# Optimization experiments

Measured on AMD Instinct MI355X. Metric: run time of the kernel, lower is better.

## Reference

```python
import jax, jax.numpy as jnp
import numpy as np

N, E, D, H = 50000, 800000, 128, 8
DH = D // H  # 16
EPS_LN = 1e-5


def layer_norm(x, gamma, beta):
    mu = jnp.mean(x, axis=-1, keepdims=True)
    var = jnp.var(x, axis=-1, keepdims=True)
    return (x - mu) * jax.lax.rsqrt(var + EPS_LN) * gamma + beta


def setup_inputs() -> dict:
    key = jax.random.key(0)
    ks = jax.random.split(key, 12)
    s = 1.0 / np.sqrt(D)
    x = jax.random.normal(ks[0], (N, D), dtype=jnp.float32)
    src = jax.random.randint(ks[1], (E,), 0, N, dtype=jnp.int32)
    dst = jax.random.randint(ks[2], (E,), 0, N, dtype=jnp.int32)
    Wq = jax.random.normal(ks[3], (D, D), dtype=jnp.float32) * s
    Wk = jax.random.normal(ks[4], (D, D), dtype=jnp.float32) * s
    Wv = jax.random.normal(ks[5], (D, D), dtype=jnp.float32) * s
    Wo = jax.random.normal(ks[6], (D, D), dtype=jnp.float32) * s
    bq = jnp.zeros((D,), jnp.float32)
    bk = jnp.zeros((D,), jnp.float32)
    bv = jnp.zeros((D,), jnp.float32)
    bo = jnp.zeros((D,), jnp.float32)
    gamma1 = jnp.ones((D,), jnp.float32)
    beta1 = jnp.zeros((D,), jnp.float32)
    gamma2 = jnp.ones((D,), jnp.float32)
    beta2 = jnp.zeros((D,), jnp.float32)
    return dict(x=x, src=src, dst=dst, Wq=Wq, bq=bq, Wk=Wk, bk=bk, Wv=Wv, bv=bv,
                Wo=Wo, bo=bo, gamma1=gamma1, beta1=beta1, gamma2=gamma2, beta2=beta2)


def reference(x, src, dst, Wq, bq, Wk, bk, Wv, bv, Wo, bo, gamma1, beta1, gamma2, beta2):
    n = x.shape[0]
    Q = (x @ Wq + bq).reshape(n, H, DH)   # [N,H,Dh]
    K = (x @ Wk + bk).reshape(n, H, DH)
    V = (x @ Wv + bv).reshape(n, H, DH)
    # edge-wise QK dot: score[e,h] = sum_d K[src[e],h,d] * Q[dst[e],h,d]
    score = jnp.sum(K[src] * Q[dst], axis=-1) / np.sqrt(DH)  # [E,H]
    score = jnp.exp(jnp.clip(score, -5.0, 5.0))
    # scatter-sum weighted values and normalizer over destination nodes
    wV = jax.ops.segment_sum(V[src] * score[..., None], dst, num_segments=n)  # [N,H,Dh]
    z = jax.ops.segment_sum(score, dst, num_segments=n)                        # [N,H]
    attn = (wV / (z[..., None] + 1e-3)).reshape(n, D)
    h = layer_norm(x + attn, gamma1, beta1)
    # sublayer: h + relu(O(LN(h)))  (dropout = 0)
    h = h + jax.nn.relu(layer_norm(h, gamma2, beta2) @ Wo + bo)
    return h
```

## Files before the change

### kernel.cpp

```cpp
#include <hip/hip_runtime.h>
#include <hip/hip_bf16.h>

typedef unsigned short ushort_t;
typedef __attribute__((ext_vector_type(8))) short short8;
typedef __attribute__((ext_vector_type(4))) float floatx4;

__device__ __forceinline__ unsigned short f2bf(float f) {
    union { float f; unsigned u; } x; x.f = f;
    unsigned r = x.u + 0x7fffu + ((x.u >> 16) & 1u);
    return (unsigned short)(r >> 16);
}
__device__ __forceinline__ float bf2f(unsigned short u) {
    union { unsigned u; float f; } x; x.u = ((unsigned)u) << 16; return x.f;
}
__device__ __forceinline__ float u2f(unsigned u) {
    union { unsigned u; float f; } x; x.u = u; return x.f;
}

__global__ __launch_bounds__(256) void transpose128(
    const float* __restrict__ Wq, const float* __restrict__ Wk,
    const float* __restrict__ Wv, const float* __restrict__ Wo,
    ushort_t* __restrict__ out)
{
    const float* W = (blockIdx.y == 0) ? Wq : (blockIdx.y == 1) ? Wk :
                     (blockIdx.y == 2) ? Wv : Wo;
    ushort_t* T = out + (size_t)blockIdx.y * 128 * 128;
    int tr = blockIdx.x >> 2, tc = blockIdx.x & 3;
    __shared__ float s[32][33];
    int tx = threadIdx.x & 31, ty = threadIdx.x >> 5;
    for (int j = 0; j < 32; j += 8)
        s[ty + j][tx] = W[(tr * 32 + ty + j) * 128 + tc * 32 + tx];
    __syncthreads();
    for (int j = 0; j < 32; j += 8)
        T[(tc * 32 + ty + j) * 128 + tr * 32 + tx] = f2bf(s[tx][ty + j]);
}

__global__ __launch_bounds__(256) void gemm_qkv(
    const float* __restrict__ X, const ushort_t* __restrict__ Wt,
    const float* __restrict__ bq, const float* __restrict__ bk, const float* __restrict__ bv,
    ushort_t* __restrict__ Q, ushort_t* __restrict__ KV, int M,
    const int* __restrict__ dst, int* __restrict__ deg, int E)
{
    __shared__ ushort_t Xs[64 * 136];
    __shared__ ushort_t Ws[128 * 136];
    int tid = threadIdx.x;
    int rowBase = blockIdx.x * 64;
    int wsel = blockIdx.y;
    const ushort_t* Wmat = Wt + (size_t)wsel * 128 * 128;
    const float* bias = (wsel == 0) ? bq : (wsel == 1) ? bk : bv;

    {
        int nblk = gridDim.x * gridDim.y;
        int fb = blockIdx.y * gridDim.x + blockIdx.x;
        int per = (E + nblk - 1) / nblk;
        int end = min(per * (fb + 1), E);
        for (int i = per * fb + tid; i < end; i += 256)
            atomicAdd(&deg[dst[i]], 1);
    }

    int r = tid >> 4;
    int c = (tid & 15) * 8;
    for (int rr = 0; rr < 64; rr += 16) {
        int row = rowBase + rr + r;
        int rc = (row < M) ? row : (M - 1);
        const float* p = X + (size_t)rc * 128 + c;
        float4 f0 = *(const float4*)p;
        float4 f1 = *(const float4*)(p + 4);
        short8 v;
        v[0] = (short)f2bf(f0.x); v[1] = (short)f2bf(f0.y);
        v[2] = (short)f2bf(f0.z); v[3] = (short)f2bf(f0.w);
        v[4] = (short)f2bf(f1.x); v[5] = (short)f2bf(f1.y);
        v[6] = (short)f2bf(f1.z); v[7] = (short)f2bf(f1.w);
        *(short8*)&Xs[(rr + r) * 136 + c] = v;
    }
    for (int rr = 0; rr < 128; rr += 16) {
        short8 v = *(const short8*)(Wmat + (size_t)(rr + r) * 128 + c);
        *(short8*)&Ws[(rr + r) * 136 + c] = v;
    }
    __syncthreads();

    int lane = tid & 63, wave = tid >> 6;
    int wm = wave * 16;
    int l15 = lane & 15, quad = lane >> 4;
    floatx4 acc[8] = {};
    for (int k0 = 0; k0 < 128; k0 += 32) {
        short8 a = *(const short8*)&Xs[(wm + l15) * 136 + k0 + quad * 8];
        for (int sn = 0; sn < 8; sn++) {
            short8 b = *(const short8*)&Ws[(sn * 16 + l15) * 136 + k0 + quad * 8];
            acc[sn] = __builtin_amdgcn_mfma_f32_16x16x32_bf16(a, b, acc[sn], 0, 0, 0);
        }
    }
    for (int sn = 0; sn < 8; sn++) {
        int col = sn * 16 + l15;
        float bia = bias[col];
        for (int rr2 = 0; rr2 < 4; rr2++) {
            int row = rowBase + wm + quad * 4 + rr2;
            if (row < M) {
                ushort_t val = f2bf(acc[sn][rr2] + bia);
                if (wsel == 0) {
                    Q[(size_t)row * 128 + col] = val;
                } else {
                    size_t idx = (size_t)row * 256 + ((col >> 3) << 4) + (col & 7) + ((wsel == 2) ? 8 : 0);
                    KV[idx] = val;
                }
            }
        }
    }
}

__global__ __launch_bounds__(256) void k_scan_blocks(const int* __restrict__ deg, int* __restrict__ offs,
                                                     int* __restrict__ bsums, int n) {
    __shared__ int s[256];
    int i = blockIdx.x * 256 + threadIdx.x;
    int v = (i < n) ? deg[i] : 0;
    s[threadIdx.x] = v;
    __syncthreads();
    for (int d = 1; d < 256; d <<= 1) {
        int t = (threadIdx.x >= d) ? s[threadIdx.x - d] : 0;
        __syncthreads();
        s[threadIdx.x] += t;
        __syncthreads();
    }
    int incl = s[threadIdx.x];
    if (i < n) offs[i] = incl - v;
    if (threadIdx.x == 255) bsums[blockIdx.x] = incl;
}

__global__ __launch_bounds__(256) void k_add_base(int* __restrict__ offs, int* __restrict__ cursor,
                                                  const int* __restrict__ bs, int nb, int n, int E) {
    int tid = threadIdx.x;
    int acc = 0;
    for (int t = tid; t < nb; t += 256)
        if (t < (int)blockIdx.x) acc += bs[t];
    for (int m = 1; m < 64; m <<= 1) acc += __shfl_xor(acc, m, 64);
    __shared__ int sw[4];
    if ((tid & 63) == 0) sw[tid >> 6] = acc;
    __syncthreads();
    int base = sw[0] + sw[1] + sw[2] + sw[3];
    int i = blockIdx.x * 256 + tid;
    if (i < n) {
        int o = offs[i] + base;
        offs[i] = o;
        cursor[i] = o;
    }
    if (blockIdx.x == 0 && tid == 0) offs[n] = E;
}

__global__ __launch_bounds__(256) void k_scatter(const int* __restrict__ src, const int* __restrict__ dst,
                                                 int* __restrict__ cursor, int* __restrict__ eadj, int E) {
    int i = blockIdx.x * 256 + threadIdx.x;
    if (i < E) {
        int p = atomicAdd(&cursor[dst[i]], 1);
        eadj[p] = src[i];
    }
}

__global__ __launch_bounds__(256) void edge_attn(
    const ushort_t* __restrict__ Qb, const ushort_t* __restrict__ KV,
    const float* __restrict__ xin,
    const int* __restrict__ offs, const int* __restrict__ eadj,
    const float* __restrict__ g1, const float* __restrict__ be1,
    const float* __restrict__ g2, const float* __restrict__ be2,
    ushort_t* __restrict__ h1out, ushort_t* __restrict__ ln2out, int N)
{
    int wave = threadIdx.x >> 6, lane = threadIdx.x & 63;
    int n = blockIdx.x * 4 + wave;
    if (n >= N) return;
    int l15 = lane & 15, grp = lane >> 4;

    uint4 qp = *(const uint4*)(Qb + (size_t)n * 128 + l15 * 8);
    float q0 = u2f(qp.x << 16), q1 = u2f(qp.x & 0xffff0000u);
    float q2 = u2f(qp.y << 16), q3 = u2f(qp.y & 0xffff0000u);
    float q4 = u2f(qp.z << 16), q5 = u2f(qp.z & 0xffff0000u);
    float q6 = u2f(qp.w << 16), q7 = u2f(qp.w & 0xffff0000u);

    int s0 = offs[n], s1 = offs[n + 1];
    float a0=0.f,a1=0.f,a2=0.f,a3=0.f,a4=0.f,a5=0.f,a6=0.f,a7=0.f,z=0.f;
    for (int base = s0; base < s1; base += 64) {
        int cnt = min(s1 - base, 64);
        int ee = (base + lane < s1) ? eadj[base + lane] : 0;
        #pragma unroll 2
        for (int j = 0; j < cnt; j += 4) {
            int jj = j + grp;
            int sn = __shfl(ee, jj, 64);
            const ushort_t* kvp = KV + (size_t)sn * 256 + l15 * 16;
            uint4 kk = *(const uint4*)kvp;
            uint4 vv = *(const uint4*)(kvp + 8);
            float d = q0 * u2f(kk.x << 16) + q1 * u2f(kk.x & 0xffff0000u)
                    + q2 * u2f(kk.y << 16) + q3 * u2f(kk.y & 0xffff0000u)
                    + q4 * u2f(kk.z << 16) + q5 * u2f(kk.z & 0xffff0000u)
                    + q6 * u2f(kk.w << 16) + q7 * u2f(kk.w & 0xffff0000u);
            d += __shfl_xor(d, 1, 64);
            float sc = fminf(5.f, fmaxf(-5.f, d * 0.25f));
            float e = (jj < cnt) ? __expf(sc) : 0.f;
            a0 = fmaf(e, u2f(vv.x << 16), a0); a1 = fmaf(e, u2f(vv.x & 0xffff0000u), a1);
            a2 = fmaf(e, u2f(vv.y << 16), a2); a3 = fmaf(e, u2f(vv.y & 0xffff0000u), a3);
            a4 = fmaf(e, u2f(vv.z << 16), a4); a5 = fmaf(e, u2f(vv.z & 0xffff0000u), a5);
            a6 = fmaf(e, u2f(vv.w << 16), a6); a7 = fmaf(e, u2f(vv.w & 0xffff0000u), a7);
            z += e;
        }
    }
    a0 += __shfl_xor(a0, 16, 64); a0 += __shfl_xor(a0, 32, 64);
    a1 += __shfl_xor(a1, 16, 64); a1 += __shfl_xor(a1, 32, 64);
    a2 += __shfl_xor(a2, 16, 64); a2 += __shfl_xor(a2, 32, 64);
    a3 += __shfl_xor(a3, 16, 64); a3 += __shfl_xor(a3, 32, 64);
    a4 += __shfl_xor(a4, 16, 64); a4 += __shfl_xor(a4, 32, 64);
    a5 += __shfl_xor(a5, 16, 64); a5 += __shfl_xor(a5, 32, 64);
    a6 += __shfl_xor(a6, 16, 64); a6 += __shfl_xor(a6, 32, 64);
    a7 += __shfl_xor(a7, 16, 64); a7 += __shfl_xor(a7, 32, 64);
    z  += __shfl_xor(z, 16, 64);  z  += __shfl_xor(z, 32, 64);
    float inv = 1.f / (z + 1e-3f);

    const float* xr = xin + (size_t)n * 128 + l15 * 8;
    float4 xa = *(const float4*)xr;
    float4 xb = *(const float4*)(xr + 4);
    float t0 = xa.x + a0 * inv, t1 = xa.y + a1 * inv;
    float t2 = xa.z + a2 * inv, t3 = xa.w + a3 * inv;
    float t4 = xb.x + a4 * inv, t5 = xb.y + a5 * inv;
    float t6 = xb.z + a6 * inv, t7 = xb.w + a7 * inv;

    float s  = t0 + t1 + t2 + t3 + t4 + t5 + t6 + t7;
    float s2 = t0*t0 + t1*t1 + t2*t2 + t3*t3 + t4*t4 + t5*t5 + t6*t6 + t7*t7;
    for (int m = 1; m < 16; m <<= 1) { s += __shfl_xor(s, m, 64); s2 += __shfl_xor(s2, m, 64); }
    float mu = s * (1.f / 128.f);
    float var = s2 * (1.f / 128.f) - mu * mu;
    float rstd = rsqrtf(var + 1e-5f);

    const float* g1r = g1 + l15 * 8;
    const float* b1r = be1 + l15 * 8;
    float4 ga = *(const float4*)g1r, gb = *(const float4*)(g1r + 4);
    float4 ba = *(const float4*)b1r, bb = *(const float4*)(b1r + 4);
    float h0 = (t0 - mu) * rstd * ga.x + ba.x;
    float h1 = (t1 - mu) * rstd * ga.y + ba.y;
    float h2 = (t2 - mu) * rstd * ga.z + ba.z;
    float h3 = (t3 - mu) * rstd * ga.w + ba.w;
    float h4 = (t4 - mu) * rstd * gb.x + bb.x;
    float h5 = (t5 - mu) * rstd * gb.y + bb.y;
    float h6 = (t6 - mu) * rstd * gb.z + bb.z;
    float h7 = (t7 - mu) * rstd * gb.w + bb.w;
    if (grp == 0) {
        uint4 pk;
        pk.x = (unsigned)f2bf(h0) | ((unsigned)f2bf(h1) << 16);
        pk.y = (unsigned)f2bf(h2) | ((unsigned)f2bf(h3) << 16);
        pk.z = (unsigned)f2bf(h4) | ((unsigned)f2bf(h5) << 16);
        pk.w = (unsigned)f2bf(h6) | ((unsigned)f2bf(h7) << 16);
        *(uint4*)(h1out + (size_t)n * 128 + l15 * 8) = pk;
    }

    s  = h0 + h1 + h2 + h3 + h4 + h5 + h6 + h7;
    s2 = h0*h0 + h1*h1 + h2*h2 + h3*h3 + h4*h4 + h5*h5 + h6*h6 + h7*h7;
    for (int m = 1; m < 16; m <<= 1) { s += __shfl_xor(s, m, 64); s2 += __shfl_xor(s2, m, 64); }
    float mu2 = s * (1.f / 128.f);
    float var2 = s2 * (1.f / 128.f) - mu2 * mu2;
    float rstd2 = rsqrtf(var2 + 1e-5f);

    const float* g2r = g2 + l15 * 8;
    const float* b2r = be2 + l15 * 8;
    float4 gc = *(const float4*)g2r, gd = *(const float4*)(g2r + 4);
    float4 bc = *(const float4*)b2r, bd = *(const float4*)(b2r + 4);
    float l0 = (h0 - mu2) * rstd2 * gc.x + bc.x;
    float l1 = (h1 - mu2) * rstd2 * gc.y + bc.y;
    float l2 = (h2 - mu2) * rstd2 * gc.z + bc.z;
    float l3 = (h3 - mu2) * rstd2 * gc.w + bc.w;
    float l4 = (h4 - mu2) * rstd2 * gd.x + bd.x;
    float l5 = (h5 - mu2) * rstd2 * gd.y + bd.y;
    float l6 = (h6 - mu2) * rstd2 * gd.z + bd.z;
    float l7 = (h7 - mu2) * rstd2 * gd.w + bd.w;
    if (grp == 1) {
        uint4 pk;
        pk.x = (unsigned)f2bf(l0) | ((unsigned)f2bf(l1) << 16);
        pk.y = (unsigned)f2bf(l2) | ((unsigned)f2bf(l3) << 16);
        pk.z = (unsigned)f2bf(l4) | ((unsigned)f2bf(l5) << 16);
        pk.w = (unsigned)f2bf(l6) | ((unsigned)f2bf(l7) << 16);
        *(uint4*)(ln2out + (size_t)n * 128 + l15 * 8) = pk;
    }
}

__global__ __launch_bounds__(256) void gemm_o(
    const ushort_t* __restrict__ X, const ushort_t* __restrict__ Wt,
    const float* __restrict__ bo, const ushort_t* __restrict__ h1in,
    float* __restrict__ Out, int M)
{
    __shared__ ushort_t As[64 * 136];
    __shared__ ushort_t Bs[64 * 136];
    int tid = threadIdx.x;
    int rowBase = blockIdx.x * 64;
    int colBase = blockIdx.y * 64;

    int r = tid >> 4;
    int c = (tid & 15) * 8;
    for (int rr = 0; rr < 64; rr += 16) {
        int row = rowBase + rr + r;
        int rc = (row < M) ? row : (M - 1);
        short8 v = *(const short8*)(X + (size_t)rc * 128 + c);
        *(short8*)&As[(rr + r) * 136 + c] = v;
    }
    for (int rr = 0; rr < 64; rr += 16) {
        short8 v = *(const short8*)(Wt + (size_t)(colBase + rr + r) * 128 + c);
        *(short8*)&Bs[(rr + r) * 136 + c] = v;
    }
    __syncthreads();

    int lane = tid & 63, wave = tid >> 6;
    int wm = (wave >> 1) * 32, wn = (wave & 1) * 32;
    int l15 = lane & 15, quad = lane >> 4;
    floatx4 acc[2][2] = {};
    for (int k0 = 0; k0 < 128; k0 += 32) {
        short8 a[2], b[2];
        for (int sm = 0; sm < 2; sm++)
            a[sm] = *(const short8*)&As[(wm + sm * 16 + l15) * 136 + k0 + quad * 8];
        for (int sn = 0; sn < 2; sn++)
            b[sn] = *(const short8*)&Bs[(wn + sn * 16 + l15) * 136 + k0 + quad * 8];
        for (int sm = 0; sm < 2; sm++)
            for (int sn = 0; sn < 2; sn++)
                acc[sm][sn] = __builtin_amdgcn_mfma_f32_16x16x32_bf16(a[sm], b[sn], acc[sm][sn], 0, 0, 0);
    }
    for (int sm = 0; sm < 2; sm++)
        for (int sn = 0; sn < 2; sn++) {
            int col = colBase + wn + sn * 16 + l15;
            float bia = bo[col];
            for (int rr2 = 0; rr2 < 4; rr2++) {
                int row = rowBase + wm + sm * 16 + quad * 4 + rr2;
                if (row < M) {
                    float v = fmaxf(acc[sm][sn][rr2] + bia, 0.f);
                    float hv = bf2f(h1in[(size_t)row * 128 + col]);
                    Out[(size_t)row * 128 + col] = hv + v;
                }
            }
        }
}

extern "C" void kernel_launch(void* const* d_in, const int* in_sizes, int n_in,
                              void* d_out, int out_size, void* d_ws, size_t ws_size,
                              hipStream_t stream) {
    const int D = 128;
    const int N = in_sizes[0] / D;
    const int E = in_sizes[1];

    const float* x   = (const float*)d_in[0];
    const int*   src = (const int*)d_in[1];
    const int*   dst = (const int*)d_in[2];
    const float* Wq  = (const float*)d_in[3];
    const float* bq  = (const float*)d_in[4];
    const float* Wk  = (const float*)d_in[5];
    const float* bk  = (const float*)d_in[6];
    const float* Wv  = (const float*)d_in[7];
    const float* bv  = (const float*)d_in[8];
    const float* Wo  = (const float*)d_in[9];
    const float* bo  = (const float*)d_in[10];
    const float* g1  = (const float*)d_in[11];
    const float* be1 = (const float*)d_in[12];
    const float* g2  = (const float*)d_in[13];
    const float* be2 = (const float*)d_in[14];

    char* ws = (char*)d_ws;
    size_t o = 0;
    auto alloc = [&](size_t b) { o = (o + 255) & ~(size_t)255; size_t r = o; o += b; return r; };
    ushort_t* Qb   = (ushort_t*)(ws + alloc((size_t)N * D * 2));
    ushort_t* KVb  = (ushort_t*)(ws + alloc((size_t)N * D * 4));
    ushort_t* ln2  = (ushort_t*)(ws + alloc((size_t)N * D * 2));
    ushort_t* h1   = (ushort_t*)(ws + alloc((size_t)N * D * 2));
    ushort_t* Wt   = (ushort_t*)(ws + alloc((size_t)4 * 128 * 128 * 2));
    int*      deg  = (int*)(ws + alloc((size_t)N * 4));
    int*      offs = (int*)(ws + alloc((size_t)(N + 1) * 4));
    int*      cur  = (int*)(ws + alloc((size_t)N * 4));
    int*      bsum = (int*)(ws + alloc((size_t)256 * 4));
    int*      eadj = (int*)(ws + alloc((size_t)E * 4));

    int nScanBlocks = (N + 255) / 256;
    int nEdgeBlocks = (E + 255) / 256;
    int nRowTiles = (N + 63) / 64;

    hipMemsetAsync(deg, 0, (size_t)N * 4, stream);
    transpose128<<<dim3(16, 4), 256, 0, stream>>>(Wq, Wk, Wv, Wo, Wt);
    gemm_qkv<<<dim3(nRowTiles, 3), 256, 0, stream>>>(x, Wt, bq, bk, bv, Qb, KVb, N, dst, deg, E);
    k_scan_blocks<<<nScanBlocks, 256, 0, stream>>>(deg, offs, bsum, N);
    k_add_base<<<nScanBlocks, 256, 0, stream>>>(offs, cur, bsum, nScanBlocks, N, E);
    k_scatter<<<nEdgeBlocks, 256, 0, stream>>>(src, dst, cur, eadj, E);
    edge_attn<<<(N + 3) / 4, 256, 0, stream>>>(Qb, KVb, x, offs, eadj, g1, be1, g2, be2, h1, ln2, N);
    gemm_o<<<dim3(nRowTiles, 2), 256, 0, stream>>>(ln2, Wt + 3 * 128 * 128, bo, h1, (float*)d_out, N);
}
```

Measured before the change: 280.6 us.

## Fuse edge attention, layer norms and output projection into one kernel

The edge attention kernel now processes 16 nodes per block (4 per wave), keeps h1 and LN2 rows in shared memory, and runs the Wo projection with MFMA directly from that tile before writing the final output. This drops the gemm_o launch and the global round trip of the bf16 h1 and ln2 buffers. Wo is read from global memory per block rather than staged, and the per-wave sequential node loop plus the block barrier may reduce latency hiding for the irregular gather. The QK dot product is also split into partial sums to shorten the dependency chain.

```diff
diff --git a/kernel.cpp b/kernel.cpp
--- a/kernel.cpp
+++ b/kernel.cpp
@@ -155,179 +155,159 @@
     }
 }
 
-__global__ __launch_bounds__(256) void edge_attn(
+__global__ __launch_bounds__(256) void attn_fused(
     const ushort_t* __restrict__ Qb, const ushort_t* __restrict__ KV,
     const float* __restrict__ xin,
     const int* __restrict__ offs, const int* __restrict__ eadj,
     const float* __restrict__ g1, const float* __restrict__ be1,
     const float* __restrict__ g2, const float* __restrict__ be2,
-    ushort_t* __restrict__ h1out, ushort_t* __restrict__ ln2out, int N)
+    const ushort_t* __restrict__ Wo_t, const float* __restrict__ bo,
+    float* __restrict__ Out, int N)
 {
+    __shared__ ushort_t ln2s[16 * 136];
+    __shared__ ushort_t h1s[16 * 136];
     int wave = threadIdx.x >> 6, lane = threadIdx.x & 63;
-    int n = blockIdx.x * 4 + wave;
-    if (n >= N) return;
     int l15 = lane & 15, grp = lane >> 4;
-
-    uint4 qp = *(const uint4*)(Qb + (size_t)n * 128 + l15 * 8);
-    float q0 = u2f(qp.x << 16), q1 = u2f(qp.x & 0xffff0000u);
-    float q2 = u2f(qp.y << 16), q3 = u2f(qp.y & 0xffff0000u);
-    float q4 = u2f(qp.z << 16), q5 = u2f(qp.z & 0xffff0000u);
-    float q6 = u2f(qp.w << 16), q7 = u2f(qp.w & 0xffff0000u);
-
-    int s0 = offs[n], s1 = offs[n + 1];
-    float a0=0.f,a1=0.f,a2=0.f,a3=0.f,a4=0.f,a5=0.f,a6=0.f,a7=0.f,z=0.f;
-    for (int base = s0; base < s1; base += 64) {
-        int cnt = min(s1 - base, 64);
-        int ee = (base + lane < s1) ? eadj[base + lane] : 0;
-        #pragma unroll 2
-        for (int j = 0; j < cnt; j += 4) {
-            int jj = j + grp;
-            int sn = __shfl(ee, jj, 64);
-            const ushort_t* kvp = KV + (size_t)sn * 256 + l15 * 16;
-            uint4 kk = *(const uint4*)kvp;
-            uint4 vv = *(const uint4*)(kvp + 8);
-            float d = q0 * u2f(kk.x << 16) + q1 * u2f(kk.x & 0xffff0000u)
-                    + q2 * u2f(kk.y << 16) + q3 * u2f(kk.y & 0xffff0000u)
-                    + q4 * u2f(kk.z << 16) + q5 * u2f(kk.z & 0xffff0000u)
-                    + q6 * u2f(kk.w << 16) + q7 * u2f(kk.w & 0xffff0000u);
-            d += __shfl_xor(d, 1, 64);
-            float sc = fminf(5.f, fmaxf(-5.f, d * 0.25f));
-            float e = (jj < cnt) ? __expf(sc) : 0.f;
-            a0 = fmaf(e, u2f(vv.x << 16), a0); a1 = fmaf(e, u2f(vv.x & 0xffff0000u), a1);
-            a2 = fmaf(e, u2f(vv.y << 16), a2); a3 = fmaf(e, u2f(vv.y & 0xffff0000u), a3);
-            a4 = fmaf(e, u2f(vv.z << 16), a4); a5 = fmaf(e, u2f(vv.z & 0xffff0000u), a5);
-            a6 = fmaf(e, u2f(vv.w << 16), a6); a7 = fmaf(e, u2f(vv.w & 0xffff0000u), a7);
-            z += e;
-        }
-    }
-    a0 += __shfl_xor(a0, 16, 64); a0 += __shfl_xor(a0, 32, 64);
-    a1 += __shfl_xor(a1, 16, 64); a1 += __shfl_xor(a1, 32, 64);
-    a2 += __shfl_xor(a2, 16, 64); a2 += __shfl_xor(a2, 32, 64);
-    a3 += __shfl_xor(a3, 16, 64); a3 += __shfl_xor(a3, 32, 64);
-    a4 += __shfl_xor(a4, 16, 64); a4 += __shfl_xor(a4, 32, 64);
-    a5 += __shfl_xor(a5, 16, 64); a5 += __shfl_xor(a5, 32, 64);
-    a6 += __shfl_xor(a6, 16, 64); a6 += __shfl_xor(a6, 32, 64);
-    a7 += __shfl_xor(a7, 16, 64); a7 += __shfl_xor(a7, 32, 64);
-    z  += __shfl_xor(z, 16, 64);  z  += __shfl_xor(z, 32, 64);
-    float inv = 1.f / (z + 1e-3f);
-
-    const float* xr = xin + (size_t)n * 128 + l15 * 8;
-    float4 xa = *(const float4*)xr;
-    float4 xb = *(const float4*)(xr + 4);
-    float t0 = xa.x + a0 * inv, t1 = xa.y + a1 * inv;
-    float t2 = xa.z + a2 * inv, t3 = xa.w + a3 * inv;
-    float t4 = xb.x + a4 * inv, t5 = xb.y + a5 * inv;
-    float t6 = xb.z + a6 * inv, t7 = xb.w + a7 * inv;
-
-    float s  = t0 + t1 + t2 + t3 + t4 + t5 + t6 + t7;
-    float s2 = t0*t0 + t1*t1 + t2*t2 + t3*t3 + t4*t4 + t5*t5 + t6*t6 + t7*t7;
-    for (int m = 1; m < 16; m <<= 1) { s += __shfl_xor(s, m, 64); s2 += __shfl_xor(s2, m, 64); }
-    float mu = s * (1.f / 128.f);
-    float var = s2 * (1.f / 128.f) - mu * mu;
-    float rstd = rsqrtf(var + 1e-5f);
-
-    const float* g1r = g1 + l15 * 8;
-    const float* b1r = be1 + l15 * 8;
-    float4 ga = *(const float4*)g1r, gb = *(const float4*)(g1r + 4);
-    float4 ba = *(const float4*)b1r, bb = *(const float4*)(b1r + 4);
-    float h0 = (t0 - mu) * rstd * ga.x + ba.x;
-    float h1 = (t1 - mu) * rstd * ga.y + ba.y;
-    float h2 = (t2 - mu) * rstd * ga.z + ba.z;
-    float h3 = (t3 - mu) * rstd * ga.w + ba.w;
-    float h4 = (t4 - mu) * rstd * gb.x + bb.x;
-    float h5 = (t5 - mu) * rstd * gb.y + bb.y;
-    float h6 = (t6 - mu) * rstd * gb.z + bb.z;
-    float h7 = (t7 - mu) * rstd * gb.w + bb.w;
-    if (grp == 0) {
-        uint4 pk;
-        pk.x = (unsigned)f2bf(h0) | ((unsigned)f2bf(h1) << 16);
-        pk.y = (unsigned)f2bf(h2) | ((unsigned)f2bf(h3) << 16);
-        pk.z = (unsigned)f2bf(h4) | ((unsigned)f2bf(h5) << 16);
-        pk.w = (unsigned)f2bf(h6) | ((unsigned)f2bf(h7) << 16);
-        *(uint4*)(h1out + (size_t)n * 128 + l15 * 8) = pk;
-    }
-
-    s  = h0 + h1 + h2 + h3 + h4 + h5 + h6 + h7;
-    s2 = h0*h0 + h1*h1 + h2*h2 + h3*h3 + h4*h4 + h5*h5 + h6*h6 + h7*h7;
-    for (int m = 1; m < 16; m <<= 1) { s += __shfl_xor(s, m, 64); s2 += __shfl_xor(s2, m, 64); }
-    float mu2 = s * (1.f / 128.f);
-    float var2 = s2 * (1.f / 128.f) - mu2 * mu2;
-    float rstd2 = rsqrtf(var2 + 1e-5f);
-
-    const float* g2r = g2 + l15 * 8;
-    const float* b2r = be2 + l15 * 8;
-    float4 gc = *(const float4*)g2r, gd = *(const float4*)(g2r + 4);
-    float4 bc = *(const float4*)b2r, bd = *(const float4*)(b2r + 4);
-    float l0 = (h0 - mu2) * rstd2 * gc.x + bc.x;
-    float l1 = (h1 - mu2) * rstd2 * gc.y + bc.y;
-    float l2 = (h2 - mu2) * rstd2 * gc.z + bc.z;
-    float l3 = (h3 - mu2) * rstd2 * gc.w + bc.w;
-    float l4 = (h4 - mu2) * rstd2 * gd.x + bd.x;
-    float l5 = (h5 - mu2) * rstd2 * gd.y + bd.y;
-    float l6 = (h6 - mu2) * rstd2 * gd.z + bd.z;
-    float l7 = (h7 - mu2) * rstd2 * gd.w + bd.w;
-    if (grp == 1) {
-        uint4 pk;
-        pk.x = (unsigned)f2bf(l0) | ((unsigned)f2bf(l1) << 16);
-        pk.y = (unsigned)f2bf(l2) | ((unsigned)f2bf(l3) << 16);
-        pk.z = (unsigned)f2bf(l4) | ((unsigned)f2bf(l5) << 16);
-        pk.w = (unsigned)f2bf(l6) | ((unsigned)f2bf(l7) << 16);
-        *(uint4*)(ln2out + (size_t)n * 128 + l15 * 8) = pk;
-    }
-}
-
-__global__ __launch_bounds__(256) void gemm_o(
-    const ushort_t* __restrict__ X, const ushort_t* __restrict__ Wt,
-    const float* __restrict__ bo, const ushort_t* __restrict__ h1in,
-    float* __restrict__ Out, int M)
-{
-    __shared__ ushort_t As[64 * 136];
-    __shared__ ushort_t Bs[64 * 136];
-    int tid = threadIdx.x;
-    int rowBase = blockIdx.x * 64;
-    int colBase = blockIdx.y * 64;
-
-    int r = tid >> 4;
-    int c = (tid & 15) * 8;
-    for (int rr = 0; rr < 64; rr += 16) {
-        int row = rowBase + rr + r;
-        int rc = (row < M) ? row : (M - 1);
-        short8 v = *(const short8*)(X + (size_t)rc * 128 + c);
-        *(short8*)&As[(rr + r) * 136 + c] = v;
-    }
-    for (int rr = 0; rr < 64; rr += 16) {
-        short8 v = *(const short8*)(Wt + (size_t)(colBase + rr + r) * 128 + c);
-        *(short8*)&Bs[(rr + r) * 136 + c] = v;
-    }
-    __syncthreads();
-
-    int lane = tid & 63, wave = tid >> 6;
-    int wm = (wave >> 1) * 32, wn = (wave & 1) * 32;
-    int l15 = lane & 15, quad = lane >> 4;
-    floatx4 acc[2][2] = {};
+    int nodeBase = blockIdx.x * 16;
+
+    for (int i = 0; i < 4; i++) {
+        int local = wave * 4 + i;
+        int n = nodeBase + local;
+        if (n >= N) break;
+
+        uint4 qp = *(const uint4*)(Qb + (size_t)n * 128 + l15 * 8);
+        float q0 = u2f(qp.x << 16), q1 = u2f(qp.x & 0xffff0000u);
+        float q2 = u2f(qp.y << 16), q3 = u2f(qp.y & 0xffff0000u);
+        float q4 = u2f(qp.z << 16), q5 = u2f(qp.z & 0xffff0000u);
+        float q6 = u2f(qp.w << 16), q7 = u2f(qp.w & 0xffff0000u);
+
+        int s0 = offs[n], s1 = offs[n + 1];
+        float a0=0.f,a1=0.f,a2=0.f,a3=0.f,a4=0.f,a5=0.f,a6=0.f,a7=0.f,z=0.f;
+        for (int base = s0; base < s1; base += 64) {
+            int cnt = min(s1 - base, 64);
+            int ee = (base + lane < s1) ? eadj[base + lane] : 0;
+            #pragma unroll 2
+            for (int j = 0; j < cnt; j += 4) {
+                int jj = j + grp;
+                int sn = __shfl(ee, jj, 64);
+                const ushort_t* kvp = KV + (size_t)sn * 256 + l15 * 16;
+                uint4 kk = *(const uint4*)kvp;
+                uint4 vv = *(const uint4*)(kvp + 8);
+                float d0 = fmaf(q1, u2f(kk.x & 0xffff0000u), q0 * u2f(kk.x << 16));
+                float d1 = fmaf(q3, u2f(kk.y & 0xffff0000u), q2 * u2f(kk.y << 16));
+                float d2 = fmaf(q5, u2f(kk.z & 0xffff0000u), q4 * u2f(kk.z << 16));
+                float d3 = fmaf(q7, u2f(kk.w & 0xffff0000u), q6 * u2f(kk.w << 16));
+                float d = (d0 + d1) + (d2 + d3);
+                d += __shfl_xor(d, 1, 64);
+                float sc = fminf(5.f, fmaxf(-5.f, d * 0.25f));
+                float e = (jj < cnt) ? __expf(sc) : 0.f;
+                a0 = fmaf(e, u2f(vv.x << 16), a0); a1 = fmaf(e, u2f(vv.x & 0xffff0000u), a1);
+                a2 = fmaf(e, u2f(vv.y << 16), a2); a3 = fmaf(e, u2f(vv.y & 0xffff0000u), a3);
+                a4 = fmaf(e, u2f(vv.z << 16), a4); a5 = fmaf(e, u2f(vv.z & 0xffff0000u), a5);
+                a6 = fmaf(e, u2f(vv.w << 16), a6); a7 = fmaf(e, u2f(vv.w & 0xffff0000u), a7);
+                z += e;
+            }
+        }
+        a0 += __shfl_xor(a0, 16, 64); a0 += __shfl_xor(a0, 32, 64);
+        a1 += __shfl_xor(a1, 16, 64); a1 += __shfl_xor(a1, 32, 64);
+        a2 += __shfl_xor(a2, 16, 64); a2 += __shfl_xor(a2, 32, 64);
+        a3 += __shfl_xor(a3, 16, 64); a3 += __shfl_xor(a3, 32, 64);
+        a4 += __shfl_xor(a4, 16, 64); a4 += __shfl_xor(a4, 32, 64);
+        a5 += __shfl_xor(a5, 16, 64); a5 += __shfl_xor(a5, 32, 64);
+        a6 += __shfl_xor(a6, 16, 64); a6 += __shfl_xor(a6, 32, 64);
+        a7 += __shfl_xor(a7, 16, 64); a7 += __shfl_xor(a7, 32, 64);
+        z  += __shfl_xor(z, 16, 64);  z  += __shfl_xor(z, 32, 64);
+        float inv = 1.f / (z + 1e-3f);
+
+        const float* xr = xin + (size_t)n * 128 + l15 * 8;
+        float4 xa = *(const float4*)xr;
+        float4 xb = *(const float4*)(xr + 4);
+        float t0 = xa.x + a0 * inv, t1 = xa.y + a1 * inv;
+        float t2 = xa.z + a2 * inv, t3 = xa.w + a3 * inv;
+        float t4 = xb.x + a4 * inv, t5 = xb.y + a5 * inv;
+        float t6 = xb.z + a6 * inv, t7 = xb.w + a7 * inv;
+
+        float s  = t0 + t1 + t2 + t3 + t4 + t5 + t6 + t7;
+        float s2 = t0*t0 + t1*t1 + t2*t2 + t3*t3 + t4*t4 + t5*t5 + t6*t6 + t7*t7;
+        for (int m = 1; m < 16; m <<= 1) { s += __shfl_xor(s, m, 64); s2 += __shfl_xor(s2, m, 64); }
+        float mu = s * (1.f / 128.f);
+        float var = s2 * (1.f / 128.f) - mu * mu;
+        float rstd = rsqrtf(var + 1e-5f);
+
+        const float* g1r = g1 + l15 * 8;
+        const float* b1r = be1 + l15 * 8;
+        float4 ga = *(const float4*)g1r, gb = *(const float4*)(g1r + 4);
+        float4 ba = *(const float4*)b1r, bb = *(const float4*)(b1r + 4);
+        float h0 = (t0 - mu) * rstd * ga.x + ba.x;
+        float h1 = (t1 - mu) * rstd * ga.y + ba.y;
+        float h2 = (t2 - mu) * rstd * ga.z + ba.z;
+        float h3 = (t3 - mu) * rstd * ga.w + ba.w;
+        float h4 = (t4 - mu) * rstd * gb.x + bb.x;
+        float h5 = (t5 - mu) * rstd * gb.y + bb.y;
+        float h6 = (t6 - mu) * rstd * gb.z + bb.z;
+        float h7 = (t7 - mu) * rstd * gb.w + bb.w;
+        if (grp == 0) {
+            uint4 pk;
+            pk.x = (unsigned)f2bf(h0) | ((unsigned)f2bf(h1) << 16);
+            pk.y = (unsigned)f2bf(h2) | ((unsigned)f2bf(h3) << 16);
+            pk.z = (unsigned)f2bf(h4) | ((unsigned)f2bf(h5) << 16);
+            pk.w = (unsigned)f2bf(h6) | ((unsigned)f2bf(h7) << 16);
+            *(uint4*)&h1s[local * 136 + l15 * 8] = pk;
+        }
+
+        s  = h0 + h1 + h2 + h3 + h4 + h5 + h6 + h7;
+        s2 = h0*h0 + h1*h1 + h2*h2 + h3*h3 + h4*h4 + h5*h5 + h6*h6 + h7*h7;
+        for (int m = 1; m < 16; m <<= 1) { s += __shfl_xor(s, m, 64); s2 += __shfl_xor(s2, m, 64); }
+        float mu2 = s * (1.f / 128.f);
+        float var2 = s2 * (1.f / 128.f) - mu2 * mu2;
+        float rstd2 = rsqrtf(var2 + 1e-5f);
+
+        const float* g2r = g2 + l15 * 8;
+        const float* b2r = be2 + l15 * 8;
+        float4 gc = *(const float4*)g2r, gd = *(const float4*)(g2r + 4);
+        float4 bc = *(const float4*)b2r, bd = *(const float4*)(b2r + 4);
+        float l0 = (h0 - mu2) * rstd2 * gc.x + bc.x;
+        float l1 = (h1 - mu2) * rstd2 * gc.y + bc.y;
+        float l2 = (h2 - mu2) * rstd2 * gc.z + bc.z;
+        float l3 = (h3 - mu2) * rstd2 * gc.w + bc.w;
+        float l4 = (h4 - mu2) * rstd2 * gd.x + bd.x;
+        float l5 = (h5 - mu2) * rstd2 * gd.y + bd.y;
+        float l6 = (h6 - mu2) * rstd2 * gd.z + bd.z;
+        float l7 = (h7 - mu2) * rstd2 * gd.w + bd.w;
+        if (grp == 1) {
+            uint4 pk;
+            pk.x = (unsigned)f2bf(l0) | ((unsigned)f2bf(l1) << 16);
+            pk.y = (unsigned)f2bf(l2) | ((unsigned)f2bf(l3) << 16);
+            pk.z = (unsigned)f2bf(l4) | ((unsigned)f2bf(l5) << 16);
+            pk.w = (unsigned)f2bf(l6) | ((unsigned)f2bf(l7) << 16);
+            *(uint4*)&ln2s[local * 136 + l15 * 8] = pk;
+        }
+    }
+    __syncthreads();
+
+    int quad = lane >> 4;
+    floatx4 acc[2] = {};
     for (int k0 = 0; k0 < 128; k0 += 32) {
-        short8 a[2], b[2];
-        for (int sm = 0; sm < 2; sm++)
-            a[sm] = *(const short8*)&As[(wm + sm * 16 + l15) * 136 + k0 + quad * 8];
-        for (int sn = 0; sn < 2; sn++)
-            b[sn] = *(const short8*)&Bs[(wn + sn * 16 + l15) * 136 + k0 + quad * 8];
-        for (int sm = 0; sm < 2; sm++)
-            for (int sn = 0; sn < 2; sn++)
-                acc[sm][sn] = __builtin_amdgcn_mfma_f32_16x16x32_bf16(a[sm], b[sn], acc[sm][sn], 0, 0, 0);
-    }
-    for (int sm = 0; sm < 2; sm++)
+        short8 a = *(const short8*)&ln2s[l15 * 136 + k0 + quad * 8];
         for (int sn = 0; sn < 2; sn++) {
-            int col = colBase + wn + sn * 16 + l15;
-            float bia = bo[col];
-            for (int rr2 = 0; rr2 < 4; rr2++) {
-                int row = rowBase + wm + sm * 16 + quad * 4 + rr2;
-                if (row < M) {
-                    float v = fmaxf(acc[sm][sn][rr2] + bia, 0.f);
-                    float hv = bf2f(h1in[(size_t)row * 128 + col]);
-                    Out[(size_t)row * 128 + col] = hv + v;
-                }
+            int col = wave * 32 + sn * 16 + l15;
+            short8 b = *(const short8*)(Wo_t + (size_t)col * 128 + k0 + quad * 8);
+            acc[sn] = __builtin_amdgcn_mfma_f32_16x16x32_bf16(a, b, acc[sn], 0, 0, 0);
+        }
+    }
+    for (int sn = 0; sn < 2; sn++) {
+        int col = wave * 32 + sn * 16 + l15;
+        float bia = bo[col];
+        for (int rr = 0; rr < 4; rr++) {
+            int rloc = quad * 4 + rr;
+            int row = nodeBase + rloc;
+            if (row < N) {
+                float v = fmaxf(acc[sn][rr] + bia, 0.f);
+                float hv = bf2f(h1s[rloc * 136 + col]);
+                Out[(size_t)row * 128 + col] = hv + v;
             }
         }
+    }
 }
 
 extern "C" void kernel_launch(void* const* d_in, const int* in_sizes, int n_in,
@@ -358,8 +338,6 @@
     auto alloc = [&](size_t b) { o = (o + 255) & ~(size_t)255; size_t r = o; o += b; return r; };
     ushort_t* Qb   = (ushort_t*)(ws + alloc((size_t)N * D * 2));
     ushort_t* KVb  = (ushort_t*)(ws + alloc((size_t)N * D * 4));
-    ushort_t* ln2  = (ushort_t*)(ws + alloc((size_t)N * D * 2));
-    ushort_t* h1   = (ushort_t*)(ws + alloc((size_t)N * D * 2));
     ushort_t* Wt   = (ushort_t*)(ws + alloc((size_t)4 * 128 * 128 * 2));
     int*      deg  = (int*)(ws + alloc((size_t)N * 4));
     int*      offs = (int*)(ws + alloc((size_t)(N + 1) * 4));
@@ -370,6 +348,7 @@
     int nScanBlocks = (N + 255) / 256;
     int nEdgeBlocks = (E + 255) / 256;
     int nRowTiles = (N + 63) / 64;
+    int nNodeBlocks = (N + 15) / 16;
 
     hipMemsetAsync(deg, 0, (size_t)N * 4, stream);
     transpose128<<<dim3(16, 4), 256, 0, stream>>>(Wq, Wk, Wv, Wo, Wt);
@@ -377,6 +356,6 @@
     k_scan_blocks<<<nScanBlocks, 256, 0, stream>>>(deg, offs, bsum, N);
     k_add_base<<<nScanBlocks, 256, 0, stream>>>(offs, cur, bsum, nScanBlocks, N, E);
     k_scatter<<<nEdgeBlocks, 256, 0, stream>>>(src, dst, cur, eadj, E);
-    edge_attn<<<(N + 3) / 4, 256, 0, stream>>>(Qb, KVb, x, offs, eadj, g1, be1, g2, be2, h1, ln2, N);
-    gemm_o<<<dim3(nRowTiles, 2), 256, 0, stream>>>(ln2, Wt + 3 * 128 * 128, bo, h1, (float*)d_out, N);
-}
+    attn_fused<<<nNodeBlocks, 256, 0, stream>>>(Qb, KVb, x, offs, eadj, g1, be1, g2, be2,
+                                                Wt + 3 * 128 * 128, bo, (float*)d_out, N);
+}
```

Measured after the change: 285.2 us. Within noise of the previous version (+1.6%).
